# Optimization experiments

Measured on AMD Instinct MI355X. Metric: run time of the kernel, lower is better.

## Reference

```python
import jax, jax.numpy as jnp
import numpy as np

B, L, H = 2, 2048, 2048
DI, N, DTR, K = 4096, 16, 128, 4  # intermediate, state, dt_rank, conv kernel


def setup_inputs() -> dict:
    key = jax.random.key(0)
    ks = jax.random.split(key, 8)
    x = jax.random.normal(ks[0], (B, L, H), jnp.float32)
    in_proj_w = jax.random.normal(ks[1], (2 * DI, H), jnp.float32) * 0.02
    conv1d_w = jax.random.normal(ks[2], (DI, 1, K), jnp.float32) * 0.1
    conv1d_b = jnp.zeros((DI,), jnp.float32)
    x_proj_w = jax.random.normal(ks[3], (DTR + 2 * N, DI), jnp.float32) * 0.02
    bound = DTR ** -0.5
    dt_proj_w = jax.random.uniform(ks[4], (DI, DTR), jnp.float32, -bound, bound)
    # faithful dt bias init: inverse-softplus of dt ~ Uniform-log[0.001, 0.1]
    dt = jnp.exp(jax.random.uniform(ks[5], (DI,), jnp.float32)
                 * (np.log(0.1) - np.log(0.001)) + np.log(0.001))
    dt = jnp.clip(dt, 1e-4)
    dt_proj_b = dt + jnp.log(-jnp.expm1(-dt))
    A_log = jnp.log(jnp.broadcast_to(jnp.arange(1, N + 1, dtype=jnp.float32), (DI, N)))
    D = jnp.ones((DI,), jnp.float32)
    out_proj_w = jax.random.normal(ks[6], (H, DI), jnp.float32) * 0.02
    return dict(x=x, in_proj_w=in_proj_w, conv1d_w=conv1d_w, conv1d_b=conv1d_b,
                x_proj_w=x_proj_w, dt_proj_w=dt_proj_w, dt_proj_b=dt_proj_b,
                A_log=A_log, D=D, out_proj_w=out_proj_w)


def _mamba_forward(x, in_proj_w, conv1d_w, conv1d_b, x_proj_w,
                   dt_proj_w, dt_proj_b, A_log, D, out_proj_w):
    # in_proj -> split into ssm input and gate (res)
    x_and_res = jnp.einsum('blh,eh->ble', x, in_proj_w)          # [B,L,2*DI]
    xi, res = jnp.split(x_and_res, 2, axis=-1)                    # [B,L,DI] each

    # depthwise causal conv1d (kernel K, left-pad K-1, truncated to L)
    xc = jnp.transpose(xi, (0, 2, 1))                             # [B,DI,L]
    xc = jax.lax.conv_general_dilated(
        xc, conv1d_w, window_strides=(1,), padding=((K - 1, 0),),
        dimension_numbers=('NCH', 'OIH', 'NCH'), feature_group_count=DI)
    xc = xc + conv1d_b[None, :, None]
    u = jax.nn.silu(jnp.transpose(xc, (0, 2, 1)))                 # [B,L,DI]

    # selective SSM parameters
    A = -jnp.exp(A_log.astype(jnp.float32))                       # [DI,N]
    x_dbl = jnp.einsum('bld,ed->ble', u, x_proj_w)                # [B,L,DTR+2N]
    dlt, Bm, Cm = jnp.split(x_dbl, [DTR, DTR + N], axis=-1)
    delta = jax.nn.softplus(jnp.einsum('blr,dr->bld', dlt, dt_proj_w) + dt_proj_b)

    # selective scan over time; carry h: [B,DI,N]
    def step(h, inp):
        d_t, B_t, C_t, u_t = inp                                  # [B,DI],[B,N],[B,N],[B,DI]
        dA = jnp.exp(d_t[:, :, None] * A)                         # [B,DI,N]
        h = dA * h + d_t[:, :, None] * B_t[:, None, :] * u_t[:, :, None]
        y_t = jnp.einsum('bdn,bn->bd', h, C_t)
        return h, y_t

    xs = (jnp.transpose(delta, (1, 0, 2)), jnp.transpose(Bm, (1, 0, 2)),
          jnp.transpose(Cm, (1, 0, 2)), jnp.transpose(u, (1, 0, 2)))
    h0 = jnp.zeros((x.shape[0], DI, N), jnp.float32)
    _, ys = jax.lax.scan(step, h0, xs)                            # ys: [L,B,DI]
    y = jnp.transpose(ys, (1, 0, 2)) + u * D.astype(jnp.float32)  # skip via D

    y = y * jax.nn.silu(res)                                      # gate
    return jnp.einsum('bld,hd->blh', y, out_proj_w)               # [B,L,H]


def reference(x, in_proj_w, conv1d_w, conv1d_b, x_proj_w,
              dt_proj_w, dt_proj_b, A_log, D, out_proj_w):
    return _mamba_forward(x, in_proj_w, conv1d_w, conv1d_b, x_proj_w,
                          dt_proj_w, dt_proj_b, A_log, D, out_proj_w)
```

## Files before the change

kernel.cpp:

```cpp
#include <hip/hip_runtime.h>
#include <hip/hip_bf16.h>
#include <stdint.h>

#define DEV static __device__ __forceinline__

typedef __attribute__((ext_vector_type(8))) short short8;
typedef __attribute__((ext_vector_type(4))) float f32x4;
typedef __attribute__((address_space(3))) void lds_void;
typedef __attribute__((address_space(1))) void glb_void;

constexpr int CB = 2, CL = 2048, CH = 2048, CDI = 4096, CN = 16, CDTR = 128;
constexpr int BLR = CB * CL;
constexpr int NC = 32, LC = 64;
constexpr int KSL = 8;

DEV ushort f2b(float f) {
  union { float f; uint32_t u; } v; v.f = f;
  uint32_t u = v.u;
  return (ushort)((u + 0x7fffu + ((u >> 16) & 1u)) >> 16);
}
DEV float b2f(ushort b) {
  union { uint32_t u; float f; } v; v.u = ((uint32_t)b) << 16;
  return v.f;
}
DEV void gload16(const ushort* g, ushort* l) {
  __builtin_amdgcn_global_load_lds((const glb_void*)g, (lds_void*)l, 16, 0, 0);
}
DEV f32x4 mfma16(short8 a, short8 b, f32x4 c) {
  return __builtin_amdgcn_mfma_f32_16x16x32_bf16(a, b, c, 0, 0, 0);
}

__global__ void cast_kernel(const float* __restrict__ in, ushort* __restrict__ out, int n4) {
  int i = blockIdx.x * blockDim.x + threadIdx.x;
  if (i >= n4) return;
  float4 v = *(const float4*)(in + (size_t)i * 4);
  *(ushort4*)(out + (size_t)i * 4) = make_ushort4(f2b(v.x), f2b(v.y), f2b(v.z), f2b(v.w));
}

__global__ void cast_pad_xproj_kernel(const float* __restrict__ in, ushort* __restrict__ out) {
  int i = blockIdx.x * blockDim.x + threadIdx.x;
  if (i >= (256 * 4096 / 4)) return;
  int idx = i * 4;
  int r = idx >> 12;
  ushort4 o;
  if (r < 160) {
    float4 v = *(const float4*)(in + idx);
    o = make_ushort4(f2b(v.x), f2b(v.y), f2b(v.z), f2b(v.w));
  } else {
    o = make_ushort4(0, 0, 0, 0);
  }
  *(ushort4*)(out + idx) = o;
}

__global__ void conv_silu_kernel(const ushort* __restrict__ xr, const float* __restrict__ w,
                                 const float* __restrict__ bias, ushort* __restrict__ u) {
  int t = blockIdx.x * blockDim.x + threadIdx.x;
  if (t >= BLR * CDI / 8) return;
  const int d8 = (t & (CDI / 8 - 1)) << 3;
  const int bl = t >> 9;
  const int l = bl & (CL - 1);
  float a[8];
  {
    float4 b0 = *(const float4*)(bias + d8);
    float4 b1 = *(const float4*)(bias + d8 + 4);
    a[0] = b0.x; a[1] = b0.y; a[2] = b0.z; a[3] = b0.w;
    a[4] = b1.x; a[5] = b1.y; a[6] = b1.z; a[7] = b1.w;
  }
  float wk[8][4];
#pragma unroll
  for (int j = 0; j < 8; ++j) {
    float4 wj = *(const float4*)(w + (size_t)(d8 + j) * 4);
    wk[j][0] = wj.x; wk[j][1] = wj.y; wk[j][2] = wj.z; wk[j][3] = wj.w;
  }
#pragma unroll
  for (int k = 0; k < 4; ++k) {
    if (l - 3 + k >= 0) {
      short8 xv = *(const short8*)(xr + (size_t)(bl - 3 + k) * 8192 + d8);
#pragma unroll
      for (int j = 0; j < 8; ++j)
        a[j] = fmaf(wk[j][k], b2f((ushort)xv[j]), a[j]);
    }
  }
  short8 o;
#pragma unroll
  for (int j = 0; j < 8; ++j) {
    float s = a[j] / (1.f + __expf(-a[j]));
    o[j] = (short)f2b(s);
  }
  *(short8*)(u + (size_t)bl * 4096 + d8) = o;
}

template<int EPI>
__global__ __launch_bounds__(256, 4)
void gemm_bt_kernel(const ushort* __restrict__ A, const ushort* __restrict__ Bw,
                    void* __restrict__ Cp, const float* __restrict__ bias,
                    int M, int N, int K) {
  __shared__ ushort sA[128 * 32];
  __shared__ ushort sB[128 * 32];
  const int tid = threadIdx.x;
  const int bm = blockIdx.x, bn = blockIdx.y;
  const int w = tid >> 6, l = tid & 63;
  const int wr = w >> 1, wc = w & 1;
  const int q = l >> 4, r = l & 15;

  f32x4 acc[4][4] = {};

  const ushort* Ab = A + (size_t)bm * 128 * K;
  const ushort* Bb = Bw + (size_t)bn * 128 * K;
  const int nk = K >> 5;
  for (int kt = 0; kt < nk; ++kt) {
    const int k0 = kt << 5;
#pragma unroll
    for (int i = 0; i < 2; ++i) {
      const int chunk = i * 256 + tid;
      const int row = chunk >> 2;
      const int cofs = (chunk & 3) << 3;
      gload16(Ab + (size_t)row * K + k0 + cofs, sA + chunk * 8);
      gload16(Bb + (size_t)row * K + k0 + cofs, sB + chunk * 8);
    }
    __syncthreads();
    short8 af[4], bfg[4];
#pragma unroll
    for (int i = 0; i < 4; ++i) {
      af[i]  = *(const short8*)(sA + (wr * 64 + i * 16 + r) * 32 + q * 8);
      bfg[i] = *(const short8*)(sB + (wc * 64 + i * 16 + r) * 32 + q * 8);
    }
#pragma unroll
    for (int i = 0; i < 4; ++i)
#pragma unroll
      for (int j = 0; j < 4; ++j)
        acc[i][j] = mfma16(af[i], bfg[j], acc[i][j]);
    __syncthreads();
  }

  const int m0 = bm * 128 + wr * 64;
  const int n0 = bn * 128 + wc * 64;
#pragma unroll
  for (int i = 0; i < 4; ++i) {
#pragma unroll
    for (int j = 0; j < 4; ++j) {
#pragma unroll
      for (int v = 0; v < 4; ++v) {
        const int grow = m0 + i * 16 + q * 4 + v;
        const int gcol = n0 + j * 16 + r;
        const float val = acc[i][j][v];
        if (EPI == 0) {
          ((ushort*)Cp)[(size_t)grow * N + gcol] = f2b(val);
        } else if (EPI == 1) {
          ((float*)Cp)[(size_t)grow * N + gcol] = val;
        } else {
          float xv = val + bias[gcol];
          float sp = xv > 20.f ? xv : log1pf(__expf(xv));
          ((ushort*)Cp)[(size_t)grow * N + gcol] = f2b(sp);
        }
      }
    }
  }
}

template<int EPI>
__global__ __launch_bounds__(512, 1)
void gemm256p_kernel(const ushort* __restrict__ A, const ushort* __restrict__ Bw,
                     void* __restrict__ Cp, int N, int K) {
  __shared__ ushort sA[2][16384];
  __shared__ ushort sB[2][16384];
  const int tid = threadIdx.x;
  const int bm = blockIdx.x, bn = blockIdx.y;
  const int wid = tid >> 6, l = tid & 63;
  const int wr = wid >> 2, wc = wid & 3;
  const int q = l >> 4, r = l & 15;
  const int rx = r & 7;
  const int nt = K >> 6;

  const ushort* Ab = A + (size_t)bm * 256 * K;
  const ushort* Bb = Bw + (size_t)bn * 256 * K;

  const int srow = tid >> 3;
  const int sxor = (tid & 7) ^ (srow & 7);

  auto stageA = [&](int T, int j) {
    const int Ts = (T < nt) ? T : (nt - 1);
    gload16(Ab + (size_t)(j * 64 + srow) * K + Ts * 64 + sxor * 8,
            &sA[T & 1][0] + j * 4096 + tid * 8);
  };
  auto stageB = [&](int T, int j) {
    const int Ts = (T < nt) ? T : (nt - 1);
    gload16(Bb + (size_t)(j * 64 + srow) * K + Ts * 64 + sxor * 8,
            &sB[T & 1][0] + j * 4096 + tid * 8);
  };

  const int sl0 = (q ^ rx) * 8;
  const int sl1 = ((4 + q) ^ rx) * 8;

  f32x4 acc[8][4] = {};

  stageA(0, 1); stageA(0, 3);
  stageB(0, 0); stageA(0, 0);
  stageB(0, 2); stageA(0, 2);
  stageB(0, 1); stageB(0, 3);
  stageA(1, 1); stageA(1, 3);
  asm volatile("s_waitcnt vmcnt(2)" ::: "memory");
  __builtin_amdgcn_s_barrier();

#define PHASE(M0, M1, S0, S1, LAST)                                        \
  {                                                                        \
    const int ra0 = (wr * 128 + (M0) * 16 + r) * 64;                       \
    const int ra1 = (wr * 128 + (M1) * 16 + r) * 64;                       \
    short8 a00 = *(const short8*)(At + ra0 + sl0);                         \
    short8 a01 = *(const short8*)(At + ra0 + sl1);                         \
    short8 a10 = *(const short8*)(At + ra1 + sl0);                         \
    short8 a11 = *(const short8*)(At + ra1 + sl1);                         \
    S0; S1;                                                                \
    if (LAST) asm volatile("s_waitcnt vmcnt(2)" ::: "memory");             \
    __builtin_amdgcn_s_barrier();                                          \
    asm volatile("s_waitcnt lgkmcnt(0)" ::: "memory");                     \
    __builtin_amdgcn_sched_barrier(0);                                     \
    __builtin_amdgcn_s_setprio(1);                                         \
    _Pragma("unroll")                                                      \
    for (int n = 0; n < 4; ++n) {                                          \
      acc[M0][n] = mfma16(a00, bf[n][0], acc[M0][n]);                      \
      acc[M0][n] = mfma16(a01, bf[n][1], acc[M0][n]);                      \
      acc[M1][n] = mfma16(a10, bf[n][0], acc[M1][n]);                      \
      acc[M1][n] = mfma16(a11, bf[n][1], acc[M1][n]);                      \
    }                                                                      \
    __builtin_amdgcn_s_setprio(0);                                         \
    __builtin_amdgcn_sched_barrier(0);                                     \
    __builtin_amdgcn_s_barrier();                                          \
  }

  for (int t = 0; t < nt; ++t) {
    const ushort* At = &sA[t & 1][0];
    const ushort* Bt = &sB[t & 1][0];
    short8 bf[4][2];
#pragma unroll
    for (int n = 0; n < 4; ++n) {
      const int br = (wc * 64 + n * 16 + r) * 64;
      bf[n][0] = *(const short8*)(Bt + br + sl0);
      bf[n][1] = *(const short8*)(Bt + br + sl1);
    }
    PHASE(6, 7, stageB(t + 1, 0), stageA(t + 1, 0), false)
    PHASE(4, 5, stageB(t + 1, 2), stageA(t + 1, 2), false)
    PHASE(2, 3, stageB(t + 1, 1), stageB(t + 1, 3), false)
    PHASE(0, 1, stageA(t + 2, 1), stageA(t + 2, 3), true)
  }
#undef PHASE

  const int m0g = bm * 256 + wr * 128;
  const int n0g = bn * 256 + wc * 64;
#pragma unroll
  for (int m = 0; m < 8; ++m)
#pragma unroll
    for (int n = 0; n < 4; ++n)
#pragma unroll
      for (int v = 0; v < 4; ++v) {
        const int grow = m0g + m * 16 + q * 4 + v;
        const int gcol = n0g + n * 16 + r;
        if (EPI == 0) ((ushort*)Cp)[(size_t)grow * N + gcol] = f2b(acc[m][n][v]);
        else          ((float*)Cp)[(size_t)grow * N + gcol]  = acc[m][n][v];
      }
}

__global__ __launch_bounds__(512, 1)
void gemm3_kernel(const ushort* __restrict__ A, const ushort* __restrict__ Bw,
                  ushort* __restrict__ Cp, const float* __restrict__ bias) {
  __shared__ ushort sA[256 * 128];
  __shared__ ushort sB[256 * 128];
  const int tid = threadIdx.x;
  const int bm = blockIdx.x, bn = blockIdx.y;
  const int wid = tid >> 6, l = tid & 63;
  const int wr = wid >> 2, wc = wid & 3;
  const int q = l >> 4, r = l & 15;

  const ushort* Ab = A + (size_t)bm * 256 * 128;
  const ushort* Bb = Bw + (size_t)bn * 256 * 128;
#pragma unroll
  for (int i = 0; i < 8; ++i) {
    const int c = i * 512 + tid;
    const int row = c >> 4, p = c & 15;
    const int lsl = p ^ (row & 7);
    gload16(Ab + (size_t)row * 128 + lsl * 8, sA + c * 8);
    gload16(Bb + (size_t)row * 128 + lsl * 8, sB + c * 8);
  }
  __syncthreads();

  f32x4 acc[8][4] = {};
  short8 bf[4][4];
#pragma unroll
  for (int n = 0; n < 4; ++n) {
    const int brow = wc * 64 + n * 16 + r;
#pragma unroll
    for (int ks = 0; ks < 4; ++ks) {
      const int p = (ks * 4 + q) ^ (brow & 7);
      bf[n][ks] = *(const short8*)(sB + brow * 128 + p * 8);
    }
  }
#pragma unroll
  for (int m = 0; m < 8; ++m) {
    const int arow = wr * 128 + m * 16 + r;
    short8 af[4];
#pragma unroll
    for (int ks = 0; ks < 4; ++ks) {
      const int p = (ks * 4 + q) ^ (arow & 7);
      af[ks] = *(const short8*)(sA + arow * 128 + p * 8);
    }
#pragma unroll
    for (int ks = 0; ks < 4; ++ks)
#pragma unroll
      for (int n = 0; n < 4; ++n)
        acc[m][n] = mfma16(af[ks], bf[n][ks], acc[m][n]);
  }

  const int m0g = bm * 256 + wr * 128;
  const int n0g = bn * 256 + wc * 64;
#pragma unroll
  for (int m = 0; m < 8; ++m)
#pragma unroll
    for (int n = 0; n < 4; ++n)
#pragma unroll
      for (int v = 0; v < 4; ++v) {
        const int grow = m0g + m * 16 + q * 4 + v;
        const int gcol = n0g + n * 16 + r;
        float xv = acc[m][n][v] + bias[gcol];
        float sp = xv > 20.f ? xv : log1pf(__expf(xv));
        Cp[(size_t)grow * 4096 + gcol] = f2b(sp);
      }
}

__global__ __launch_bounds__(256, 4)
void gemm_btk_kernel(const ushort* __restrict__ A, const ushort* __restrict__ Bw,
                     float* __restrict__ Cpart, int N, int Ktot, int Ksl) {
  __shared__ ushort sA[128 * 32];
  __shared__ ushort sB[128 * 32];
  const int tid = threadIdx.x;
  const int bm = blockIdx.x, bn = blockIdx.y, z = blockIdx.z;
  const int w = tid >> 6, l = tid & 63;
  const int wr = w >> 1, wc = w & 1;
  const int q = l >> 4, r = l & 15;

  f32x4 acc[4][4] = {};

  const ushort* Ab = A + (size_t)bm * 128 * Ktot + z * Ksl;
  const ushort* Bb = Bw + (size_t)bn * 128 * Ktot + z * Ksl;
  const int nk = Ksl >> 5;
  for (int kt = 0; kt < nk; ++kt) {
    const int k0 = kt << 5;
#pragma unroll
    for (int i = 0; i < 2; ++i) {
      const int chunk = i * 256 + tid;
      const int row = chunk >> 2;
      const int cofs = (chunk & 3) << 3;
      gload16(Ab + (size_t)row * Ktot + k0 + cofs, sA + chunk * 8);
      gload16(Bb + (size_t)row * Ktot + k0 + cofs, sB + chunk * 8);
    }
    __syncthreads();
    short8 af[4], bfg[4];
#pragma unroll
    for (int i = 0; i < 4; ++i) {
      af[i]  = *(const short8*)(sA + (wr * 64 + i * 16 + r) * 32 + q * 8);
      bfg[i] = *(const short8*)(sB + (wc * 64 + i * 16 + r) * 32 + q * 8);
    }
#pragma unroll
    for (int i = 0; i < 4; ++i)
#pragma unroll
      for (int j = 0; j < 4; ++j)
        acc[i][j] = mfma16(af[i], bfg[j], acc[i][j]);
    __syncthreads();
  }

  float* Cz = Cpart + (size_t)z * BLR * N;
  const int m0 = bm * 128 + wr * 64;
  const int n0 = bn * 128 + wc * 64;
#pragma unroll
  for (int i = 0; i < 4; ++i)
#pragma unroll
    for (int j = 0; j < 4; ++j)
#pragma unroll
      for (int v = 0; v < 4; ++v)
        Cz[(size_t)(m0 + i * 16 + q * 4 + v) * N + (n0 + j * 16 + r)] = acc[i][j][v];
}

__global__ __launch_bounds__(256)
void reduce_xdbl_kernel(const float* __restrict__ part, float* __restrict__ xdbl,
                        ushort* __restrict__ dlt) {
  const int i = blockIdx.x * 256 + threadIdx.x;
  const int idx = i * 4;
  const int row = idx >> 8, col = idx & 255;
  float4 s = make_float4(0.f, 0.f, 0.f, 0.f);
#pragma unroll
  for (int z = 0; z < KSL; ++z) {
    float4 v = *(const float4*)(part + (size_t)z * BLR * 256 + idx);
    s.x += v.x; s.y += v.y; s.z += v.z; s.w += v.w;
  }
  *(float4*)(xdbl + idx) = s;
  if (col < 128) {
    *(ushort4*)(dlt + (size_t)row * 128 + col) =
        make_ushort4(f2b(s.x), f2b(s.y), f2b(s.z), f2b(s.w));
  }
}

__global__ __launch_bounds__(256)
void scan_pass1_kernel(const ushort* __restrict__ delta_bf, const ushort* __restrict__ u_bf,
                       const float* __restrict__ xdbl, const float* __restrict__ A_log,
                       float* __restrict__ Hc, float* __restrict__ Ssum) {
  __shared__ float4 sB[LC * 4];
  const int blk = blockIdx.x;
  const int dblk = blk & 15, bc = blk >> 4;
  const int b = bc & (CB - 1), c = bc >> 1;
  const int tid = threadIdx.x;
  const int d = dblk * 256 + tid;
  const size_t rowbase = (size_t)b * CL + c * LC;

  {
    const int rr = tid >> 2, seg = tid & 3;
    sB[tid] = *(const float4*)(xdbl + (rowbase + rr) * 256 + 128 + seg * 4);
  }
  __syncthreads();

  float Ae[16];
#pragma unroll
  for (int n = 0; n < 16; ++n) Ae[n] = -__expf(A_log[(size_t)d * CN + n]);
  float h[16] = {};
  float S = 0.f;
  for (int t = 0; t < LC; ++t) {
    const float dl = b2f(delta_bf[(rowbase + t) * 4096 + d]);
    const float uu = b2f(u_bf[(rowbase + t) * 4096 + d]);
    const float du = dl * uu;
    S += dl;
#pragma unroll
    for (int q = 0; q < 4; ++q) {
      float4 bq = sB[t * 4 + q];
      h[q * 4 + 0] = __expf(Ae[q * 4 + 0] * dl) * h[q * 4 + 0] + du * bq.x;
      h[q * 4 + 1] = __expf(Ae[q * 4 + 1] * dl) * h[q * 4 + 1] + du * bq.y;
      h[q * 4 + 2] = __expf(Ae[q * 4 + 2] * dl) * h[q * 4 + 2] + du * bq.z;
      h[q * 4 + 3] = __expf(Ae[q * 4 + 3] * dl) * h[q * 4 + 3] + du * bq.w;
    }
  }
  float4* Hp = (float4*)(Hc + ((((size_t)c * CB + b) * CDI + d) << 4));
#pragma unroll
  for (int q = 0; q < 4; ++q)
    Hp[q] = make_float4(h[q * 4 + 0], h[q * 4 + 1], h[q * 4 + 2], h[q * 4 + 3]);
  Ssum[((size_t)c * CB + b) * CDI + d] = S;
}

__global__ __launch_bounds__(256)
void scan_pass2_kernel(float* __restrict__ Hc, const float* __restrict__ Ssum,
                       const float* __restrict__ A_log) {
  const int t = blockIdx.x * 256 + threadIdx.x;
  const int n = t & 15, d = (t >> 4) & (CDI - 1), b = t >> 16;
  const float Ae = -__expf(A_log[(size_t)d * CN + n]);
  float h = 0.f;
  for (int c = 1; c < NC; ++c) {
    const size_t idxp = ((size_t)(c - 1) * CB + b) * CDI + d;
    const float P = __expf(Ae * Ssum[idxp]);
    h = P * h + Hc[idxp * 16 + n];
    Hc[idxp * 16 + n] = h;
  }
}

__global__ __launch_bounds__(256)
void scan_pass3_kernel(const ushort* __restrict__ delta_bf, const ushort* __restrict__ u_bf,
                       const float* __restrict__ xdbl, const ushort* __restrict__ xr,
                       const float* __restrict__ A_log, const float* __restrict__ Dvec,
                       const float* __restrict__ Hc, ushort* __restrict__ ybf) {
  __shared__ float4 sB[LC * 4];
  __shared__ float4 sC[LC * 4];
  const int blk = blockIdx.x;
  const int dblk = blk & 15, bc = blk >> 4;
  const int b = bc & (CB - 1), c = bc >> 1;
  const int tid = threadIdx.x;
  const int d = dblk * 256 + tid;
  const size_t rowbase = (size_t)b * CL + c * LC;

  {
    const int rr = tid >> 2, seg = tid & 3;
    sB[tid] = *(const float4*)(xdbl + (rowbase + rr) * 256 + 128 + seg * 4);
    sC[tid] = *(const float4*)(xdbl + (rowbase + rr) * 256 + 144 + seg * 4);
  }
  __syncthreads();

  float Ae[16];
#pragma unroll
  for (int n = 0; n < 16; ++n) Ae[n] = -__expf(A_log[(size_t)d * CN + n]);
  float h[16];
  if (c == 0) {
#pragma unroll
    for (int n = 0; n < 16; ++n) h[n] = 0.f;
  } else {
    const float4* Hp = (const float4*)(Hc + ((((size_t)(c - 1) * CB + b) * CDI + d) << 4));
#pragma unroll
    for (int q = 0; q < 4; ++q) {
      float4 hv = Hp[q];
      h[q * 4 + 0] = hv.x; h[q * 4 + 1] = hv.y; h[q * 4 + 2] = hv.z; h[q * 4 + 3] = hv.w;
    }
  }
  const float Dd = Dvec[d];
  for (int t = 0; t < LC; ++t) {
    const float dl = b2f(delta_bf[(rowbase + t) * 4096 + d]);
    const float uu = b2f(u_bf[(rowbase + t) * 4096 + d]);
    const float du = dl * uu;
    float y = 0.f;
#pragma unroll
    for (int q = 0; q < 4; ++q) {
      float4 bq = sB[t * 4 + q];
      float4 cq = sC[t * 4 + q];
      h[q * 4 + 0] = __expf(Ae[q * 4 + 0] * dl) * h[q * 4 + 0] + du * bq.x;
      h[q * 4 + 1] = __expf(Ae[q * 4 + 1] * dl) * h[q * 4 + 1] + du * bq.y;
      h[q * 4 + 2] = __expf(Ae[q * 4 + 2] * dl) * h[q * 4 + 2] + du * bq.z;
      h[q * 4 + 3] = __expf(Ae[q * 4 + 3] * dl) * h[q * 4 + 3] + du * bq.w;
      y = fmaf(h[q * 4 + 0], cq.x, y);
      y = fmaf(h[q * 4 + 1], cq.y, y);
      y = fmaf(h[q * 4 + 2], cq.z, y);
      y = fmaf(h[q * 4 + 3], cq.w, y);
    }
    const float res = b2f(xr[(rowbase + t) * 8192 + 4096 + d]);
    const float sres = res / (1.f + __expf(-res));
    ybf[(rowbase + t) * 4096 + d] = f2b((y + uu * Dd) * sres);
  }
}

extern "C" void kernel_launch(void* const* d_in, const int* in_sizes, int n_in,
                              void* d_out, int out_size, void* d_ws, size_t ws_size,
                              hipStream_t stream) {
  (void)in_sizes; (void)n_in; (void)out_size; (void)ws_size;
  const float* x       = (const float*)d_in[0];
  const float* in_w    = (const float*)d_in[1];
  const float* conv_w  = (const float*)d_in[2];
  const float* conv_b  = (const float*)d_in[3];
  const float* xproj_w = (const float*)d_in[4];
  const float* dt_w    = (const float*)d_in[5];
  const float* dt_b    = (const float*)d_in[6];
  const float* A_log   = (const float*)d_in[7];
  const float* Dvec    = (const float*)d_in[8];
  const float* out_w   = (const float*)d_in[9];
  float* out = (float*)d_out;
  char* ws = (char*)d_ws;
  const size_t MB = 1u << 20;

  ushort* xb    = (ushort*)(ws);
  float*  Hc    = (float*)(ws);
  ushort* wout  = (ushort*)(ws);
  ushort* wb1   = (ushort*)(ws + 16 * MB);
  ushort* u_bf  = (ushort*)(ws + 16 * MB);
  ushort* xr    = (ushort*)(ws + 48 * MB);
  float*  part  = (float*)(ws + 112 * MB);
  ushort* delta = (ushort*)(ws + 112 * MB);
  ushort* ybf   = (ushort*)(ws + 144 * MB);
  float*  xdbl  = (float*)(ws + 176 * MB);
  ushort* dlt   = (ushort*)(ws + 180 * MB);
  ushort* wxp   = (ushort*)(ws + 181 * MB);
  ushort* wdt   = (ushort*)(ws + 183 * MB);
  float*  Ssum  = (float*)(ws + 184 * MB);

  auto cast = [&](const float* in, ushort* o, int n) {
    cast_kernel<<<(n / 4 + 255) / 256, 256, 0, stream>>>(in, o, n / 4);
  };

  cast(x, xb, BLR * CH);
  cast(in_w, wb1, 2 * CDI * CH);
  gemm256p_kernel<0><<<dim3(BLR / 256, (2 * CDI) / 256), 512, 0, stream>>>(
      xb, wb1, xr, 2 * CDI, CH);
  conv_silu_kernel<<<(BLR * CDI / 8) / 256, 256, 0, stream>>>(xr, conv_w, conv_b, u_bf);
  cast_pad_xproj_kernel<<<(256 * 4096 / 4) / 256, 256, 0, stream>>>(xproj_w, wxp);
  gemm_btk_kernel<<<dim3(BLR / 128, 2, KSL), 256, 0, stream>>>(
      u_bf, wxp, part, 256, CDI, CDI / KSL);
  reduce_xdbl_kernel<<<(BLR * 256 / 4) / 256, 256, 0, stream>>>(part, xdbl, dlt);
  cast(dt_w, wdt, CDI * CDTR);
  gemm3_kernel<<<dim3(BLR / 256, CDI / 256), 512, 0, stream>>>(dlt, wdt, delta, dt_b);
  scan_pass1_kernel<<<NC * CB * (CDI / 256), 256, 0, stream>>>(
      delta, u_bf, xdbl, A_log, Hc, Ssum);
  scan_pass2_kernel<<<(CB * CDI * CN) / 256, 256, 0, stream>>>(Hc, Ssum, A_log);
  scan_pass3_kernel<<<NC * CB * (CDI / 256), 256, 0, stream>>>(
      delta, u_bf, xdbl, xr, A_log, Dvec, Hc, ybf);
  cast(out_w, wout, CH * CDI);
  gemm_bt_kernel<1><<<dim3(BLR / 128, CH / 128), 256, 0, stream>>>(
      ybf, wout, out, nullptr, BLR, CH, CDI);
}
```

Before: 556.0 us.

## Use triple-buffered 128x256 MFMA GEMM kernel for out_proj

Replaces the generic 128x128 gemm_bt kernel for the output projection with a new 512-thread kernel that computes 128x256 tiles. It stages A and B into three LDS buffers using direct global-to-LDS loads and splits each K step into two half-phases, interleaving the next tile's loads with the MFMAs and raising wave priority during compute. This is meant to hide memory latency and increase per-block reuse, at the cost of half as many blocks (256 for the 4096x2048 output) and heavy LDS use.

```diff
diff --git a/kernel.cpp b/kernel.cpp
--- a/kernel.cpp
+++ b/kernel.cpp
@@ -260,6 +260,126 @@
       }
 }
 
+template<int EPI>
+__global__ __launch_bounds__(512, 1)
+void gemm128x256_kernel(const ushort* __restrict__ A, const ushort* __restrict__ Bw,
+                        void* __restrict__ Cp, int N, int K) {
+  __shared__ ushort sA[3][8192];
+  __shared__ ushort sB[3][16384];
+  const int tid = threadIdx.x;
+  const int bm = blockIdx.x, bn = blockIdx.y;
+  const int wid = tid >> 6, l = tid & 63;
+  const int wr = wid >> 2, wc = wid & 3;
+  const int q = l >> 4, r = l & 15;
+  const int rx = r & 7;
+  const int nt = K >> 6;
+
+  const ushort* Ab = A + (size_t)bm * 128 * K;
+  const ushort* Bb = Bw + (size_t)bn * 256 * K;
+
+  const int srow = tid >> 3;
+  const int sxor = (tid & 7) ^ (srow & 7);
+
+  auto stageA = [&](int T, int buf, int j) {
+    const int Ts = (T < nt) ? T : (nt - 1);
+    gload16(Ab + (size_t)(j * 64 + srow) * K + Ts * 64 + sxor * 8,
+            &sA[buf][0] + j * 4096 + tid * 8);
+  };
+  auto stageB = [&](int T, int buf, int j) {
+    const int Ts = (T < nt) ? T : (nt - 1);
+    gload16(Bb + (size_t)(j * 64 + srow) * K + Ts * 64 + sxor * 8,
+            &sB[buf][0] + j * 4096 + tid * 8);
+  };
+
+  const int sl0 = (q ^ rx) * 8;
+  const int sl1 = ((4 + q) ^ rx) * 8;
+
+  f32x4 acc[4][4] = {};
+
+  stageA(0, 0, 0); stageA(0, 0, 1);
+  stageB(0, 0, 0); stageB(0, 0, 1); stageB(0, 0, 2); stageB(0, 0, 3);
+  stageA(1, 1, 0); stageA(1, 1, 1);
+  asm volatile("s_waitcnt vmcnt(2)" ::: "memory");
+  __builtin_amdgcn_s_barrier();
+
+  int c0 = 0;
+  for (int t = 0; t < nt; ++t) {
+    const int c1 = (c0 == 2) ? 0 : c0 + 1;
+    const int c2 = (c1 == 2) ? 0 : c1 + 1;
+    const ushort* At = &sA[c0][0];
+    const ushort* Bt = &sB[c0][0];
+    short8 bf[4][2];
+#pragma unroll
+    for (int n = 0; n < 4; ++n) {
+      const int br = (wc * 64 + n * 16 + r) * 64;
+      bf[n][0] = *(const short8*)(Bt + br + sl0);
+      bf[n][1] = *(const short8*)(Bt + br + sl1);
+    }
+    {
+      const int ra0 = (wr * 64 + 2 * 16 + r) * 64;
+      const int ra1 = (wr * 64 + 3 * 16 + r) * 64;
+      short8 a00 = *(const short8*)(At + ra0 + sl0);
+      short8 a01 = *(const short8*)(At + ra0 + sl1);
+      short8 a10 = *(const short8*)(At + ra1 + sl0);
+      short8 a11 = *(const short8*)(At + ra1 + sl1);
+      stageB(t + 1, c1, 0); stageB(t + 1, c1, 1); stageB(t + 1, c1, 2);
+      __builtin_amdgcn_s_barrier();
+      asm volatile("s_waitcnt lgkmcnt(0)" ::: "memory");
+      __builtin_amdgcn_sched_barrier(0);
+      __builtin_amdgcn_s_setprio(1);
+#pragma unroll
+      for (int n = 0; n < 4; ++n) {
+        acc[2][n] = mfma16(a00, bf[n][0], acc[2][n]);
+        acc[2][n] = mfma16(a01, bf[n][1], acc[2][n]);
+        acc[3][n] = mfma16(a10, bf[n][0], acc[3][n]);
+        acc[3][n] = mfma16(a11, bf[n][1], acc[3][n]);
+      }
+      __builtin_amdgcn_s_setprio(0);
+      __builtin_amdgcn_sched_barrier(0);
+      __builtin_amdgcn_s_barrier();
+    }
+    {
+      const int ra0 = (wr * 64 + 0 * 16 + r) * 64;
+      const int ra1 = (wr * 64 + 1 * 16 + r) * 64;
+      short8 a00 = *(const short8*)(At + ra0 + sl0);
+      short8 a01 = *(const short8*)(At + ra0 + sl1);
+      short8 a10 = *(const short8*)(At + ra1 + sl0);
+      short8 a11 = *(const short8*)(At + ra1 + sl1);
+      stageB(t + 1, c1, 3); stageA(t + 2, c2, 0); stageA(t + 2, c2, 1);
+      asm volatile("s_waitcnt vmcnt(2)" ::: "memory");
+      __builtin_amdgcn_s_barrier();
+      asm volatile("s_waitcnt lgkmcnt(0)" ::: "memory");
+      __builtin_amdgcn_sched_barrier(0);
+      __builtin_amdgcn_s_setprio(1);
+#pragma unroll
+      for (int n = 0; n < 4; ++n) {
+        acc[0][n] = mfma16(a00, bf[n][0], acc[0][n]);
+        acc[0][n] = mfma16(a01, bf[n][1], acc[0][n]);
+        acc[1][n] = mfma16(a10, bf[n][0], acc[1][n]);
+        acc[1][n] = mfma16(a11, bf[n][1], acc[1][n]);
+      }
+      __builtin_amdgcn_s_setprio(0);
+      __builtin_amdgcn_sched_barrier(0);
+      __builtin_amdgcn_s_barrier();
+    }
+    c0 = c1;
+  }
+
+  const int m0g = bm * 128 + wr * 64;
+  const int n0g = bn * 256 + wc * 64;
+#pragma unroll
+  for (int m = 0; m < 4; ++m)
+#pragma unroll
+    for (int n = 0; n < 4; ++n)
+#pragma unroll
+      for (int v = 0; v < 4; ++v) {
+        const int grow = m0g + m * 16 + q * 4 + v;
+        const int gcol = n0g + n * 16 + r;
+        if (EPI == 0) ((ushort*)Cp)[(size_t)grow * N + gcol] = f2b(acc[m][n][v]);
+        else          ((float*)Cp)[(size_t)grow * N + gcol]  = acc[m][n][v];
+      }
+}
+
 __global__ __launch_bounds__(512, 1)
 void gemm3_kernel(const ushort* __restrict__ A, const ushort* __restrict__ Bw,
                   ushort* __restrict__ Cp, const float* __restrict__ bias) {
@@ -572,6 +692,6 @@
   scan_pass3_kernel<<<NC * CB * (CDI / 256), 256, 0, stream>>>(
       delta, u_bf, xdbl, xr, A_log, Dvec, Hc, ybf);
   cast(out_w, wout, CH * CDI);
-  gemm_bt_kernel<1><<<dim3(BLR / 128, CH / 128), 256, 0, stream>>>(
-      ybf, wout, out, nullptr, BLR, CH, CDI);
-}
+  gemm128x256_kernel<1><<<dim3(BLR / 128, CH / 256), 512, 0, stream>>>(
+      ybf, wout, out, CH, CDI);
+}
```

Result: no change. 549.1 us (-1.2%).
